# Optimization experiments

Measured on AMD Instinct MI355X. Metric: run time of the kernel, lower is better.

Reference implementation:

```python
import jax, jax.numpy as jnp
import numpy as np


def _apply_1q(state, U, wire):
    # state: (B,) + (2,)*n big-endian (wire 0 = axis 1, Pennylane convention)
    # U: (2,2) shared or (B,2,2) per-sample
    s = jnp.moveaxis(state, wire + 1, 1)
    eq = 'bij,bj...->bi...' if U.ndim == 3 else 'ij,bj...->bi...'
    s = jnp.einsum(eq, U, s)
    return jnp.moveaxis(s, 1, wire + 1)


def _rx(theta):  # theta: (B,) -> (B,2,2)
    c = jnp.cos(theta / 2).astype(jnp.complex64)
    s = (-1j * jnp.sin(theta / 2)).astype(jnp.complex64)
    return jnp.stack([jnp.stack([c, s], -1), jnp.stack([s, c], -1)], -2)


def _ry(theta):  # theta: (B,) -> (B,2,2)
    c = jnp.cos(theta / 2).astype(jnp.complex64)
    s = jnp.sin(theta / 2).astype(jnp.complex64)
    return jnp.stack([jnp.stack([c, -s], -1), jnp.stack([s, c], -1)], -2)


def _rot(phi, theta, omega):  # Pennylane Rot = RZ(omega) RY(theta) RZ(phi)
    c = jnp.cos(theta / 2)
    s = jnp.sin(theta / 2)
    r0 = jnp.stack([jnp.exp(-1j * (phi + omega) / 2) * c,
                    -jnp.exp(1j * (phi - omega) / 2) * s])
    r1 = jnp.stack([jnp.exp(-1j * (phi - omega) / 2) * s,
                    jnp.exp(1j * (phi + omega) / 2) * c])
    return jnp.stack([r0, r1]).astype(jnp.complex64)


def _cnot_adj(state, ctrl):
    # CNOT(control=ctrl, target=ctrl+1): flip target axis on control=1 slice
    a0 = jax.lax.index_in_dim(state, 0, ctrl + 1, keepdims=True)
    a1 = jax.lax.index_in_dim(state, 1, ctrl + 1, keepdims=True)
    return jnp.concatenate([a0, jnp.flip(a1, axis=ctrl + 2)], axis=ctrl + 1)


def _forward(state_batch, weights, head_w, head_b):
    L, n, _ = weights.shape
    B = state_batch.shape[0]
    psi = jnp.zeros((B, 2 ** n), jnp.complex64).at[:, 0].set(1.0)
    psi = psi.reshape((B,) + (2,) * n)
    # angle encoding (only first two features are used, as in the torch module)
    psi = _apply_1q(psi, _rx(state_batch[:, 0]), 0)
    psi = _apply_1q(psi, _ry(state_batch[:, 1]), 1)
    for l in range(L):
        for w in range(n):
            psi = _apply_1q(psi, _rot(weights[l, w, 0], weights[l, w, 1], weights[l, w, 2]), w)
        for i in range(n - 1):
            psi = _cnot_adj(psi, i)
    probs = psi.real ** 2 + psi.imag ** 2  # (B,) + (2,)*n
    feats = []
    for w in range(n):  # expval PauliZ on each wire
        p = probs.sum(axis=tuple(a for a in range(1, n + 1) if a != w + 1))
        feats.append(p[:, 0] - p[:, 1])
    features = jnp.stack(feats, axis=-1)  # (B, n)
    return (features @ head_w.T + head_b).squeeze(-1)  # (B,)


def setup_inputs() -> dict:
    key = jax.random.key(0)
    k1, k2, k3 = jax.random.split(key, 3)
    B, n, L = 8192, 12, 8
    return {
        'state_batch': jax.random.normal(k1, (B, 8), jnp.float32),
        'weights': jax.random.normal(k2, (L, n, 3), jnp.float32),
        'head_w': jax.random.normal(k3, (1, n), jnp.float32) / np.float32(np.sqrt(n)),
        'head_b': jnp.zeros((1,), jnp.float32),
    }


def reference(state_batch, weights, head_w, head_b):
    return _forward(state_batch, weights, head_w, head_b)
```

## Files before the change

kernel.cpp:

```cpp
#include <hip/hip_runtime.h>
#include <hip/hip_fp16.h>


typedef __half2 h2;
struct Gate32 { float a, b, c, d; };

__device__ __forceinline__ float bpermf(int addr4, float v) {
    return __int_as_float(__builtin_amdgcn_ds_bpermute(addr4, __float_as_int(v)));
}
__device__ __forceinline__ h2 bperm2(int addr4, h2 v) {
    int x = __builtin_amdgcn_ds_bpermute(addr4, __builtin_bit_cast(int, v));
    return __builtin_bit_cast(h2, x);
}
__device__ __forceinline__ int ginv9(int y) {
    y ^= y >> 1; y ^= y >> 2; y ^= y >> 4; y ^= y >> 8;
    return y & 511;
}
__device__ __forceinline__ h2 sp(float x) {
    return __half2half2(__float2half(x));
}
__device__ __forceinline__ h2 rot16(h2 v) {
    unsigned u = __builtin_bit_cast(unsigned, v);
    u = (u << 16) | (u >> 16);
    return __builtin_bit_cast(h2, u);
}

struct H2C { h2 a, b, c, d, nb, nc, nd; };
__device__ __forceinline__ void reg_pair(h2& a0r, h2& a0i, h2& a1r, h2& a1i,
                                         const H2C& R) {
    const h2 x0r = a0r, x0i = a0i, x1r = a1r, x1i = a1i;
    a0r = __hfma2(R.d,  x1i, __hfma2(R.nc, x1r, __hfma2(R.b,  x0i, __hmul2(R.a, x0r))));
    a0i = __hfma2(R.nd, x1r, __hfma2(R.nc, x1i, __hfma2(R.nb, x0r, __hmul2(R.a, x0i))));
    a1r = __hfma2(R.nb, x1i, __hfma2(R.a,  x1r, __hfma2(R.d,  x0i, __hmul2(R.c, x0r))));
    a1i = __hfma2(R.b,  x1r, __hfma2(R.a,  x1i, __hfma2(R.nd, x0r, __hmul2(R.c, x0i))));
}

__global__ __launch_bounds__(512, 1)
void sim_kernel(const float* __restrict__ wts, float2* __restrict__ cols) {
    const int t = threadIdx.x;
    const int b = blockIdx.x;

    __shared__ Gate32 gt[96];
    __shared__ h2 xb[2][512 * 10];
    if (t < 96) {
        const int l = t / 12, w = t % 12;
        const float* lw = wts + l*36 + w*3;
        const float phi = lw[0], th = lw[1], om = lw[2];
        float ch, sh, ca, sa, cb, sb;
        __sincosf(0.5f*th,       &sh, &ch);
        __sincosf(0.5f*(phi+om), &sa, &ca);
        __sincosf(0.5f*(phi-om), &sb, &cb);
        Gate32 r; r.a = ca*ch; r.b = sa*ch; r.c = cb*sh; r.d = sb*sh;
        gt[t] = r;
    }

    h2 ar2[4], ai2[4];
    const h2 zero = sp(0.f);
#pragma unroll
    for (int k = 0; k < 4; ++k) { ar2[k] = zero; ai2[k] = zero; }
    if (t == (b << 7)) ar2[0] = __halves2half2(__float2half(1.f), __float2half(0.f));

    int p = t;
    int Minv[9] = {1, 2, 4, 8, 16, 32, 64, 128, 256};

    __syncthreads();

#pragma unroll 1
    for (int l = 0; l < 8; ++l) {
        const int base = l * 12;
#pragma unroll
        for (int w = 0; w < 3; ++w) {
            const Gate32 R = gt[base + w];
            const int pb = 8 - w;
            const bool bs = (p >> pb) & 1;
            const h2 A2   = sp(R.a);
            const h2 csi2 = sp(bs ? R.b : -R.b);
            const h2 ncsi2 = __hneg2(csi2);
            const h2 cor2 = sp(bs ? R.c : -R.c);
            const h2 D2   = sp(R.d);
            const h2 nD2  = __hneg2(D2);
            h2* buf = xb[(l*3 + w) & 1];
            h2* own = buf + t * 10;
#pragma unroll
            for (int k = 0; k < 4; ++k) {
                const h2 u = __hfma2(nD2, ai2[k], __hmul2(cor2, ar2[k]));
                const h2 v = __hfma2(D2,  ar2[k], __hmul2(cor2, ai2[k]));
                reinterpret_cast<int2*>(own)[k] =
                    make_int2(__builtin_bit_cast(int, u),
                              __builtin_bit_cast(int, v));
            }
            __syncthreads();
            const h2* par = buf + (t ^ Minv[pb]) * 10;
            int2 q[4];
#pragma unroll
            for (int k = 0; k < 4; ++k)
                q[k] = reinterpret_cast<const int2*>(par)[k];
#pragma unroll
            for (int k = 0; k < 4; ++k) {
                const h2 U = __builtin_bit_cast(h2, q[k].x);
                const h2 V = __builtin_bit_cast(h2, q[k].y);
                const h2 nr = __hsub2(__hfma2(ncsi2, ai2[k], __hmul2(A2, ar2[k])), U);
                const h2 ni = __hsub2(__hfma2(csi2,  ar2[k], __hmul2(A2, ai2[k])), V);
                ar2[k] = nr; ai2[k] = ni;
            }
        }
#pragma unroll
        for (int w = 3; w < 9; ++w) {
            const Gate32 R = gt[base + w];
            const int pb = 8 - w;
            const bool bs = (p >> pb) & 1;
            const h2 A2   = sp(R.a);
            const h2 csi2 = sp(bs ? R.b : -R.b);
            const h2 ncsi2 = __hneg2(csi2);
            const h2 cor2 = sp(bs ? R.c : -R.c);
            const h2 D2   = sp(R.d);
            const h2 nD2  = __hneg2(D2);
            const int addr4 = ((t & 63) ^ Minv[pb]) << 2;
            h2 u[4], v[4];
#pragma unroll
            for (int k = 0; k < 4; ++k) {
                u[k] = __hfma2(nD2, ai2[k], __hmul2(cor2, ar2[k]));
                v[k] = __hfma2(D2,  ar2[k], __hmul2(cor2, ai2[k]));
            }
            h2 U[4], V[4];
#pragma unroll
            for (int k = 0; k < 4; ++k) {
                U[k] = bperm2(addr4, u[k]);
                V[k] = bperm2(addr4, v[k]);
            }
#pragma unroll
            for (int k = 0; k < 4; ++k) {
                const h2 nr = __hsub2(__hfma2(ncsi2, ai2[k], __hmul2(A2, ar2[k])), U[k]);
                const h2 ni = __hsub2(__hfma2(csi2,  ar2[k], __hmul2(A2, ai2[k])), V[k]);
                ar2[k] = nr; ai2[k] = ni;
            }
        }
        {
            const Gate32 R = gt[base + 9];
            H2C C; C.a = sp(R.a); C.b = sp(R.b); C.c = sp(R.c); C.d = sp(R.d);
            C.nb = __hneg2(C.b); C.nc = __hneg2(C.c); C.nd = __hneg2(C.d);
            reg_pair(ar2[0], ai2[0], ar2[2], ai2[2], C);
            reg_pair(ar2[1], ai2[1], ar2[3], ai2[3], C);
        }
        {
            const Gate32 R = gt[base + 10];
            H2C C; C.a = sp(R.a); C.b = sp(R.b); C.c = sp(R.c); C.d = sp(R.d);
            C.nb = __hneg2(C.b); C.nc = __hneg2(C.c); C.nd = __hneg2(C.d);
            reg_pair(ar2[0], ai2[0], ar2[1], ai2[1], C);
            reg_pair(ar2[2], ai2[2], ar2[3], ai2[3], C);
        }
        {
            const Gate32 R = gt[base + 11];
            const h2 cP  = __halves2half2(__float2half( R.a), __float2half( R.c));
            const h2 cQ  = __halves2half2(__float2half( R.b), __float2half( R.d));
            const h2 cR  = __halves2half2(__float2half(-R.c), __float2half( R.a));
            const h2 cS  = __halves2half2(__float2half( R.d), __float2half(-R.b));
            const h2 cQn = __hneg2(cQ);
            const h2 cSn = __hneg2(cS);
#pragma unroll
            for (int k = 0; k < 4; ++k) {
                const h2 arv = ar2[k], aiv = ai2[k];
                const h2 arx = __low2half2(arv), ary = __high2half2(arv);
                const h2 aix = __low2half2(aiv), aiy = __high2half2(aiv);
                ar2[k] = __hfma2(cS,  aiy, __hfma2(cR, ary, __hfma2(cQ,  aix, __hmul2(cP, arx))));
                ai2[k] = __hfma2(cSn, ary, __hfma2(cR, aiy, __hfma2(cQn, arx, __hmul2(cP, aix))));
            }
        }
        const int c = __popc(p) & 1;
        {
            h2 t0;
            t0 = ar2[0]; ar2[0] = c ? ar2[2] : ar2[0]; ar2[2] = c ? t0 : ar2[2];
            t0 = ar2[1]; ar2[1] = c ? ar2[3] : ar2[1]; ar2[3] = c ? t0 : ar2[3];
            t0 = ai2[0]; ai2[0] = c ? ai2[2] : ai2[0]; ai2[2] = c ? t0 : ai2[2];
            t0 = ai2[1]; ai2[1] = c ? ai2[3] : ai2[1]; ai2[3] = c ? t0 : ai2[3];
            h2 tmp = ar2[2]; ar2[2] = ar2[3]; ar2[3] = rot16(tmp);
            ar2[1] = rot16(ar2[1]);
            tmp = ai2[2]; ai2[2] = ai2[3]; ai2[3] = rot16(tmp);
            ai2[1] = rot16(ai2[1]);
        }
        p = ginv9(p);
#pragma unroll
        for (int pb = 8; pb >= 1; --pb) Minv[pb] ^= Minv[pb-1];
    }

    float4* dst4 = reinterpret_cast<float4*>(cols + b*4096 + (p << 3));
#pragma unroll
    for (int k = 0; k < 4; ++k)
        dst4[k] = make_float4(__low2float(ar2[k]),  __low2float(ai2[k]),
                              __high2float(ar2[k]), __high2float(ai2[k]));
}

__global__ __launch_bounds__(256)
void finish_kernel(const float* __restrict__ sb,
                   const float2* __restrict__ cols,
                   const float* __restrict__ hw,
                   const float* __restrict__ hb,
                   float* __restrict__ out, int B) {
    const int tid  = threadIdx.x;
    const int lane = tid & 63, wid = tid >> 6;

    float hwv[12];
#pragma unroll
    for (int w = 0; w < 12; ++w) hwv[w] = hw[w];

    float Klo = 0.f;
#pragma unroll
    for (int w = 4; w < 12; ++w)
        Klo += ((tid >> (11 - w)) & 1) ? -hwv[w] : hwv[w];

    float g[10];
#pragma unroll
    for (int m = 0; m < 10; ++m) g[m] = 0.f;

#pragma unroll 1
    for (int it = 0; it < 16; ++it) {
        const int q = (it << 8) | tid;
        const float2 c0 = cols[q];
        const float2 c1 = cols[4096  + q];
        const float2 c2 = cols[8192  + q];
        const float2 c3 = cols[12288 + q];
        float K = Klo;
#pragma unroll
        for (int w = 0; w < 4; ++w)
            K += ((it >> (3 - w)) & 1) ? -hwv[w] : hwv[w];
        g[0] += K * (c0.x*c0.x + c0.y*c0.y);
        g[1] += K * (c1.x*c1.x + c1.y*c1.y);
        g[2] += K * (c2.x*c2.x + c2.y*c2.y);
        g[3] += K * (c3.x*c3.x + c3.y*c3.y);
        g[4] += K * (c0.x*c1.x + c0.y*c1.y);
        g[5] += K * (c2.x*c3.x + c2.y*c3.y);
        g[6] += K * (c0.x*c2.y - c0.y*c2.x);
        g[7] += K * (c0.x*c3.y - c0.y*c3.x);
        g[8] += K * (c1.x*c2.y - c1.y*c2.x);
        g[9] += K * (c1.x*c3.y - c1.y*c3.x);
    }

    __shared__ float gsh[4][10];
#pragma unroll
    for (int m = 0; m < 10; ++m) {
#pragma unroll
        for (int off = 1; off < 64; off <<= 1)
            g[m] += bpermf((lane ^ off) << 2, g[m]);
    }
    if (lane == 0) {
#pragma unroll
        for (int m = 0; m < 10; ++m) gsh[wid][m] = g[m];
    }
    __syncthreads();
    float G[10];
#pragma unroll
    for (int m = 0; m < 10; ++m) {
        const float s = gsh[0][m] + gsh[1][m] + gsh[2][m] + gsh[3][m];
        G[m] = (m < 4) ? s : 2.f * s;
    }

    const int i = blockIdx.x * 256 + tid;
    if (i < B) {
        const float2 x = *reinterpret_cast<const float2*>(sb + i*8);
        float c0, s0, c1, s1;
        __sincosf(0.5f * x.x, &s0, &c0);
        __sincosf(0.5f * x.y, &s1, &c1);
        const float a0 = c0*c1, a1 = c0*s1, a2 = s0*c1, a3 = s0*s1;
        const float r = G[0]*a0*a0 + G[1]*a1*a1 + G[2]*a2*a2 + G[3]*a3*a3
                      + G[4]*(a0*a1) + G[5]*(a2*a3)
                      + G[6]*(a0*a2) + G[7]*(a0*a3)
                      + G[8]*(a1*a2) + G[9]*(a1*a3);
        out[i] = r + hb[0];
    }
}

extern "C" void kernel_launch(void* const* d_in, const int* in_sizes, int n_in,
                              void* d_out, int out_size, void* d_ws, size_t ws_size,
                              hipStream_t stream) {
    const float* sb  = (const float*)d_in[0];
    const float* wts = (const float*)d_in[1];
    const float* hw  = (const float*)d_in[2];
    const float* hb  = (const float*)d_in[3];
    float* out = (float*)d_out;
    float2* cols = (float2*)d_ws;
    const int B = in_sizes[0] / 8;
    sim_kernel   <<<4, 512, 0, stream>>>(wts, cols);
    finish_kernel<<<(B + 255)/256, 256, 0, stream>>>(sb, cols, hw, hb, out, B);
}
```

Before: 92.21 us.

## Precompute half2 gate coefficients in separate kernel and widen LDS exchange

Moves the per-gate trig and coefficient setup out of the simulation kernel into a small prologue kernel that writes pre-packed half2 coefficients (with sign flips done by XOR masks) to workspace. The sim kernel reads gates straight from global memory, drops its initial barrier, and exchanges partner amplitudes through 16-byte LDS stores and loads instead of 8-byte ones. The aim is to cut per-gate float-to-half conversion and LDS instruction count. In exchange it adds a third kernel launch, and the coefficient loads now go through global memory or cache instead of LDS.

```diff
diff --git a/kernel.cpp b/kernel.cpp
--- a/kernel.cpp
+++ b/kernel.cpp
@@ -3,7 +3,7 @@
 
 
 typedef __half2 h2;
-struct Gate32 { float a, b, c, d; };
+struct GateRecH2 { h2 a2, b2, c2, d2; };
 
 __device__ __forceinline__ float bpermf(int addr4, float v) {
     return __int_as_float(__builtin_amdgcn_ds_bpermute(addr4, __float_as_int(v)));
@@ -24,6 +24,9 @@
     u = (u << 16) | (u >> 16);
     return __builtin_bit_cast(h2, u);
 }
+__device__ __forceinline__ h2 bch2(int x)  { return __builtin_bit_cast(h2, x); }
+__device__ __forceinline__ int bci(h2 x)   { return __builtin_bit_cast(int, x); }
+#define NEGMASK 0x80008000
 
 struct H2C { h2 a, b, c, d, nb, nc, nd; };
 __device__ __forceinline__ void reg_pair(h2& a0r, h2& a0i, h2& a1r, h2& a1i,
@@ -35,25 +38,37 @@
     a1i = __hfma2(R.b,  x1r, __hfma2(R.a,  x1i, __hfma2(R.nd, x0r, __hmul2(R.c, x0i))));
 }
 
+__global__ void coeff_kernel(const float* __restrict__ wts,
+                             GateRecH2* __restrict__ tbl,
+                             h2* __restrict__ w11) {
+    const int g = threadIdx.x;
+    if (g >= 96) return;
+    const int l = g / 12, w = g % 12;
+    const float* lw = wts + l*36 + w*3;
+    const float phi = lw[0], th = lw[1], om = lw[2];
+    float ch, sh, ca, sa, cb, sb;
+    __sincosf(0.5f*th,       &sh, &ch);
+    __sincosf(0.5f*(phi+om), &sa, &ca);
+    __sincosf(0.5f*(phi-om), &sb, &cb);
+    const float A = ca*ch, B = sa*ch, C = cb*sh, D = sb*sh;
+    GateRecH2 r; r.a2 = sp(A); r.b2 = sp(B); r.c2 = sp(C); r.d2 = sp(D);
+    tbl[g] = r;
+    if (w == 11) {
+        w11[l*4 + 0] = __halves2half2(__float2half( A), __float2half( C));
+        w11[l*4 + 1] = __halves2half2(__float2half( B), __float2half( D));
+        w11[l*4 + 2] = __halves2half2(__float2half(-C), __float2half( A));
+        w11[l*4 + 3] = __halves2half2(__float2half( D), __float2half(-B));
+    }
+}
+
 __global__ __launch_bounds__(512, 1)
-void sim_kernel(const float* __restrict__ wts, float2* __restrict__ cols) {
+void sim_kernel(const GateRecH2* __restrict__ tbl,
+                const h2* __restrict__ w11,
+                float2* __restrict__ cols) {
     const int t = threadIdx.x;
     const int b = blockIdx.x;
 
-    __shared__ Gate32 gt[96];
-    __shared__ h2 xb[2][512 * 10];
-    if (t < 96) {
-        const int l = t / 12, w = t % 12;
-        const float* lw = wts + l*36 + w*3;
-        const float phi = lw[0], th = lw[1], om = lw[2];
-        float ch, sh, ca, sa, cb, sb;
-        __sincosf(0.5f*th,       &sh, &ch);
-        __sincosf(0.5f*(phi+om), &sa, &ca);
-        __sincosf(0.5f*(phi-om), &sb, &cb);
-        Gate32 r; r.a = ca*ch; r.b = sa*ch; r.c = cb*sh; r.d = sb*sh;
-        gt[t] = r;
-    }
-
+    __shared__ int4 xb[2][512 * 3];
     h2 ar2[4], ai2[4];
     const h2 zero = sp(0.f);
 #pragma unroll
@@ -62,59 +77,57 @@
 
     int p = t;
     int Minv[9] = {1, 2, 4, 8, 16, 32, 64, 128, 256};
-
-    __syncthreads();
 
 #pragma unroll 1
     for (int l = 0; l < 8; ++l) {
         const int base = l * 12;
 #pragma unroll
         for (int w = 0; w < 3; ++w) {
-            const Gate32 R = gt[base + w];
+            const int4 rv = *reinterpret_cast<const int4*>(tbl + base + w);
             const int pb = 8 - w;
             const bool bs = (p >> pb) & 1;
-            const h2 A2   = sp(R.a);
-            const h2 csi2 = sp(bs ? R.b : -R.b);
-            const h2 ncsi2 = __hneg2(csi2);
-            const h2 cor2 = sp(bs ? R.c : -R.c);
-            const h2 D2   = sp(R.d);
-            const h2 nD2  = __hneg2(D2);
-            h2* buf = xb[(l*3 + w) & 1];
-            h2* own = buf + t * 10;
-#pragma unroll
-            for (int k = 0; k < 4; ++k) {
-                const h2 u = __hfma2(nD2, ai2[k], __hmul2(cor2, ar2[k]));
-                const h2 v = __hfma2(D2,  ar2[k], __hmul2(cor2, ai2[k]));
-                reinterpret_cast<int2*>(own)[k] =
-                    make_int2(__builtin_bit_cast(int, u),
-                              __builtin_bit_cast(int, v));
-            }
+            const h2 A2    = bch2(rv.x);
+            const int bi   = bs ? rv.y : (rv.y ^ NEGMASK);
+            const h2 csi2  = bch2(bi);
+            const h2 ncsi2 = bch2(bi ^ NEGMASK);
+            const h2 cor2  = bch2(bs ? rv.z : (rv.z ^ NEGMASK));
+            const h2 D2    = bch2(rv.w);
+            const h2 nD2   = bch2(rv.w ^ NEGMASK);
+            int4* buf = xb[(l*3 + w) & 1];
+            h2 u[4], v[4];
+#pragma unroll
+            for (int k = 0; k < 4; ++k) {
+                u[k] = __hfma2(nD2, ai2[k], __hmul2(cor2, ar2[k]));
+                v[k] = __hfma2(D2,  ar2[k], __hmul2(cor2, ai2[k]));
+            }
+            int4* own = buf + t * 3;
+            own[0] = make_int4(bci(u[0]), bci(u[1]), bci(u[2]), bci(u[3]));
+            own[1] = make_int4(bci(v[0]), bci(v[1]), bci(v[2]), bci(v[3]));
             __syncthreads();
-            const h2* par = buf + (t ^ Minv[pb]) * 10;
-            int2 q[4];
-#pragma unroll
-            for (int k = 0; k < 4; ++k)
-                q[k] = reinterpret_cast<const int2*>(par)[k];
-#pragma unroll
-            for (int k = 0; k < 4; ++k) {
-                const h2 U = __builtin_bit_cast(h2, q[k].x);
-                const h2 V = __builtin_bit_cast(h2, q[k].y);
-                const h2 nr = __hsub2(__hfma2(ncsi2, ai2[k], __hmul2(A2, ar2[k])), U);
-                const h2 ni = __hsub2(__hfma2(csi2,  ar2[k], __hmul2(A2, ai2[k])), V);
+            const int4* par = buf + (t ^ Minv[pb]) * 3;
+            const int4 qu = par[0];
+            const int4 qv = par[1];
+            const int U[4] = {qu.x, qu.y, qu.z, qu.w};
+            const int V[4] = {qv.x, qv.y, qv.z, qv.w};
+#pragma unroll
+            for (int k = 0; k < 4; ++k) {
+                const h2 nr = __hsub2(__hfma2(ncsi2, ai2[k], __hmul2(A2, ar2[k])), bch2(U[k]));
+                const h2 ni = __hsub2(__hfma2(csi2,  ar2[k], __hmul2(A2, ai2[k])), bch2(V[k]));
                 ar2[k] = nr; ai2[k] = ni;
             }
         }
 #pragma unroll
         for (int w = 3; w < 9; ++w) {
-            const Gate32 R = gt[base + w];
+            const int4 rv = *reinterpret_cast<const int4*>(tbl + base + w);
             const int pb = 8 - w;
             const bool bs = (p >> pb) & 1;
-            const h2 A2   = sp(R.a);
-            const h2 csi2 = sp(bs ? R.b : -R.b);
-            const h2 ncsi2 = __hneg2(csi2);
-            const h2 cor2 = sp(bs ? R.c : -R.c);
-            const h2 D2   = sp(R.d);
-            const h2 nD2  = __hneg2(D2);
+            const h2 A2    = bch2(rv.x);
+            const int bi   = bs ? rv.y : (rv.y ^ NEGMASK);
+            const h2 csi2  = bch2(bi);
+            const h2 ncsi2 = bch2(bi ^ NEGMASK);
+            const h2 cor2  = bch2(bs ? rv.z : (rv.z ^ NEGMASK));
+            const h2 D2    = bch2(rv.w);
+            const h2 nD2   = bch2(rv.w ^ NEGMASK);
             const int addr4 = ((t & 63) ^ Minv[pb]) << 2;
             h2 u[4], v[4];
 #pragma unroll
@@ -136,27 +149,27 @@
             }
         }
         {
-            const Gate32 R = gt[base + 9];
-            H2C C; C.a = sp(R.a); C.b = sp(R.b); C.c = sp(R.c); C.d = sp(R.d);
-            C.nb = __hneg2(C.b); C.nc = __hneg2(C.c); C.nd = __hneg2(C.d);
+            const int4 rv = *reinterpret_cast<const int4*>(tbl + base + 9);
+            H2C C; C.a = bch2(rv.x); C.b = bch2(rv.y); C.c = bch2(rv.z); C.d = bch2(rv.w);
+            C.nb = bch2(rv.y ^ NEGMASK); C.nc = bch2(rv.z ^ NEGMASK); C.nd = bch2(rv.w ^ NEGMASK);
             reg_pair(ar2[0], ai2[0], ar2[2], ai2[2], C);
             reg_pair(ar2[1], ai2[1], ar2[3], ai2[3], C);
         }
         {
-            const Gate32 R = gt[base + 10];
-            H2C C; C.a = sp(R.a); C.b = sp(R.b); C.c = sp(R.c); C.d = sp(R.d);
-            C.nb = __hneg2(C.b); C.nc = __hneg2(C.c); C.nd = __hneg2(C.d);
+            const int4 rv = *reinterpret_cast<const int4*>(tbl + base + 10);
+            H2C C; C.a = bch2(rv.x); C.b = bch2(rv.y); C.c = bch2(rv.z); C.d = bch2(rv.w);
+            C.nb = bch2(rv.y ^ NEGMASK); C.nc = bch2(rv.z ^ NEGMASK); C.nd = bch2(rv.w ^ NEGMASK);
             reg_pair(ar2[0], ai2[0], ar2[1], ai2[1], C);
             reg_pair(ar2[2], ai2[2], ar2[3], ai2[3], C);
         }
         {
-            const Gate32 R = gt[base + 11];
-            const h2 cP  = __halves2half2(__float2half( R.a), __float2half( R.c));
-            const h2 cQ  = __halves2half2(__float2half( R.b), __float2half( R.d));
-            const h2 cR  = __halves2half2(__float2half(-R.c), __float2half( R.a));
-            const h2 cS  = __halves2half2(__float2half( R.d), __float2half(-R.b));
-            const h2 cQn = __hneg2(cQ);
-            const h2 cSn = __hneg2(cS);
+            const int4 wv = *reinterpret_cast<const int4*>(w11 + l*4);
+            const h2 cP  = bch2(wv.x);
+            const h2 cQ  = bch2(wv.y);
+            const h2 cR  = bch2(wv.z);
+            const h2 cS  = bch2(wv.w);
+            const h2 cQn = bch2(wv.y ^ NEGMASK);
+            const h2 cSn = bch2(wv.w ^ NEGMASK);
 #pragma unroll
             for (int k = 0; k < 4; ++k) {
                 const h2 arv = ar2[k], aiv = ai2[k];
@@ -277,8 +290,11 @@
     const float* hw  = (const float*)d_in[2];
     const float* hb  = (const float*)d_in[3];
     float* out = (float*)d_out;
-    float2* cols = (float2*)d_ws;
+    GateRecH2* tbl = (GateRecH2*)d_ws;
+    h2* w11 = (h2*)((char*)d_ws + 1536);
+    float2* cols = (float2*)((char*)d_ws + 4096);
     const int B = in_sizes[0] / 8;
-    sim_kernel   <<<4, 512, 0, stream>>>(wts, cols);
+    coeff_kernel <<<1, 128, 0, stream>>>(wts, tbl, w11);
+    sim_kernel   <<<4, 512, 0, stream>>>(tbl, w11, cols);
     finish_kernel<<<(B + 255)/256, 256, 0, stream>>>(sb, cols, hw, hb, out, B);
 }
```

Result: slower. 94.10 us (+2.1%).
